# Kernel optimization log

Measured on AMD Instinct MI355X. Metric: run time of the kernel, lower is better.

The kernel has to match this reference:

```python
import jax, jax.numpy as jnp
import numpy as np

B, T, D, H, E, TOPK = 4, 1024, 1024, 16, 8, 2
DH = D // H
FF = 4 * D
EPS = 1e-9


def setup_inputs() -> dict:
    key = jax.random.key(0)
    ks = jax.random.split(key, 8)
    s = 0.02
    return {
        "x": jax.random.normal(ks[0], (B, T, D), jnp.float32),
        "c": jax.random.normal(ks[1], (B, 1, D), jnp.float32),
        "ln1_w": jnp.ones((D,), jnp.float32),
        "w_qkv": jax.random.normal(ks[2], (3 * D, D), jnp.float32) * s,
        "w_proj": jax.random.normal(ks[3], (D, D), jnp.float32) * s,
        "ln2_w": jnp.ones((D,), jnp.float32),
        "router_w": jax.random.normal(ks[4], (E, D), jnp.float32) * s,
        "expert_w1": jax.random.normal(ks[5], (E, FF, D), jnp.float32) * s,
        "expert_w2": jax.random.normal(ks[6], (E, D, FF), jnp.float32) * s,
    }


def _layernorm(x, w):
    mu = jnp.mean(x, axis=-1, keepdims=True)
    var = jnp.mean(jnp.square(x - mu), axis=-1, keepdims=True)
    return (x - mu) * jax.lax.rsqrt(var + 1e-5) * w


def reference(x, c, ln1_w, w_qkv, w_proj, ln2_w, router_w, expert_w1, expert_w2):
    # --- causal self-attention with AdaLN-style additive conditioning ---
    h = _layernorm(x, ln1_w) + c                          # [B,T,D]
    qkv = jnp.einsum('btd,ed->bte', h, w_qkv)             # [B,T,3D]
    q, k, v = jnp.split(qkv, 3, axis=-1)
    q = q.reshape(B, T, H, DH).transpose(0, 2, 1, 3)       # [B,H,T,dh]
    k = k.reshape(B, T, H, DH).transpose(0, 2, 1, 3)
    v = v.reshape(B, T, H, DH).transpose(0, 2, 1, 3)
    scores = jnp.einsum('bhqd,bhkd->bhqk', q, k) / jnp.sqrt(jnp.float32(DH))
    causal = jnp.tril(jnp.ones((T, T), bool))
    scores = jnp.where(causal, scores, jnp.float32(-1e30))
    attn = jax.nn.softmax(scores, axis=-1)
    o = jnp.einsum('bhqk,bhkd->bhqd', attn, v)
    o = o.transpose(0, 2, 1, 3).reshape(B, T, D)
    x = x + jnp.einsum('btd,ed->bte', o, w_proj)

    # --- pre-MoE LayerNorm (note: module overwrites x with ln_2(x)) ---
    x = _layernorm(x, ln2_w)

    # --- router (non-cond path): linear, max-shift, softmax, eps clamp, top-k ---
    logits = jnp.einsum('btd,ed->bte', x, router_w)        # [B,T,E]
    logits = logits - jnp.max(logits, axis=-1, keepdims=True)
    probs = jax.nn.softmax(logits, axis=-1)
    probs = jnp.clip(probs + EPS, EPS, 1.0 - EPS)
    _, top_idx = jax.lax.top_k(probs, TOPK)                # [B,T,k]
    mask = jnp.sum(jax.nn.one_hot(top_idx, E, dtype=probs.dtype), axis=-2)  # [B,T,E]
    router_probs = mask * probs
    router_probs = router_probs / jnp.sum(router_probs, axis=-1, keepdims=True)

    # --- experts: GPT MLP per expert (fc -> GELU -> proj), combine by probs ---
    # Dense-compute form is mathematically identical: router_probs is 0 for
    # non-selected experts, so masked gather/scatter == weighted dense sum.
    hid = jax.nn.gelu(jnp.einsum('btd,efd->btef', x, expert_w1), approximate=False)
    expert_out = jnp.einsum('btef,edf->bted', hid, expert_w2)  # [B,T,E,D]
    next_states = jnp.einsum('bted,bte->btd', expert_out, router_probs)

    return x + next_states
```

## Files before the change

kernel.cpp:

```cpp
#include <hip/hip_runtime.h>
#include <cstdint>
#include <cstddef>


#define AS1 __attribute__((address_space(1)))
#define AS3 __attribute__((address_space(3)))

typedef unsigned short u16;
typedef __attribute__((ext_vector_type(8))) short short8;
typedef __attribute__((ext_vector_type(8))) _Float16 half8;
typedef __attribute__((ext_vector_type(4))) float f32x4;

constexpr int Bc = 4, Tc = 1024, Dc = 1024, Hc = 16, Ec = 8, FFc = 4096;
constexpr int Mtok = Bc * Tc;

constexpr size_t PS_WQKV = (size_t)3 * Dc * Dc;
constexpr size_t PS_WPROJ = (size_t)Dc * Dc;
constexpr size_t PS_H = (size_t)Mtok * Dc;

constexpr float LO_SCALE = 4096.0f;
constexpr float LO_INV = 1.0f / 4096.0f;

__device__ __forceinline__ u16 f2bf(float f) {
  unsigned u = __float_as_uint(f);
  u += 0x7fffu + ((u >> 16) & 1u);
  return (u16)(u >> 16);
}
__device__ __forceinline__ float bf2f(u16 v) { return __uint_as_float(((unsigned)v) << 16); }
__device__ __forceinline__ u16 f2h(float f) {
  _Float16 h = (_Float16)f;
  return *(u16*)&h;
}
__device__ __forceinline__ float h2f(u16 v) {
  _Float16 h = *(_Float16*)&v;
  return (float)h;
}
__device__ __forceinline__ float gelu_f(float v) {
  return 0.5f * v * (1.0f + erff(v * 0.70710678118654752440f));
}

__global__ __launch_bounds__(256) void cvt_fp16_kernel(const float* __restrict__ in,
                                                       u16* __restrict__ out, int n4) {
  int i = blockIdx.x * 256 + threadIdx.x;
  if (i >= n4) return;
  float4 v = reinterpret_cast<const float4*>(in)[i];
  uint2 o;
  o.x = (unsigned)f2h(v.x) | ((unsigned)f2h(v.y) << 16);
  o.y = (unsigned)f2h(v.z) | ((unsigned)f2h(v.w) << 16);
  reinterpret_cast<uint2*>(out)[i] = o;
}

__global__ __launch_bounds__(256) void split2h_kernel(const float* __restrict__ in,
                                                      u16* __restrict__ out,
                                                      size_t ps, int n4) {
  int i = blockIdx.x * 256 + threadIdx.x;
  if (i >= n4) return;
  float4 v = reinterpret_cast<const float4*>(in)[i];
  float a[4] = {v.x, v.y, v.z, v.w};
  unsigned h[4], lo[4];
#pragma unroll
  for (int j = 0; j < 4; ++j) {
    u16 hh = f2h(a[j]);
    float r = (a[j] - h2f(hh)) * LO_SCALE;
    h[j] = hh; lo[j] = f2h(r);
  }
  uint2 o0, o1;
  o0.x = h[0] | (h[1] << 16);   o0.y = h[2] | (h[3] << 16);
  o1.x = lo[0] | (lo[1] << 16); o1.y = lo[2] | (lo[3] << 16);
  const size_t base = (size_t)i * 4;
  *(uint2*)&out[base] = o0;
  *(uint2*)&out[ps + base] = o1;
}

__global__ __launch_bounds__(256) void ln1_kernel(const float* __restrict__ x,
                                                  const float* __restrict__ w,
                                                  const float* __restrict__ c,
                                                  u16* __restrict__ hp) {
  const int row = blockIdx.x, tid = threadIdx.x;
  const int b = row >> 10;
  const float4 v = reinterpret_cast<const float4*>(x + (size_t)row * Dc)[tid];
  __shared__ float red[256];
  red[tid] = v.x + v.y + v.z + v.w;
  __syncthreads();
  for (int s = 128; s > 0; s >>= 1) { if (tid < s) red[tid] += red[tid + s]; __syncthreads(); }
  const float mu = red[0] * (1.0f / Dc);
  __syncthreads();
  const float dx = v.x - mu, dy = v.y - mu, dz = v.z - mu, dw = v.w - mu;
  red[tid] = dx * dx + dy * dy + dz * dz + dw * dw;
  __syncthreads();
  for (int s = 128; s > 0; s >>= 1) { if (tid < s) red[tid] += red[tid + s]; __syncthreads(); }
  const float rs = rsqrtf(red[0] * (1.0f / Dc) + 1e-5f);
  const float4 wv = reinterpret_cast<const float4*>(w)[tid];
  const float4 cv = reinterpret_cast<const float4*>(c + (size_t)b * Dc)[tid];
  float a[4];
  a[0] = dx * rs * wv.x + cv.x; a[1] = dy * rs * wv.y + cv.y;
  a[2] = dz * rs * wv.z + cv.z; a[3] = dw * rs * wv.w + cv.w;
  unsigned h[4], lo[4];
#pragma unroll
  for (int j = 0; j < 4; ++j) {
    u16 hh = f2h(a[j]);
    float r = (a[j] - h2f(hh)) * LO_SCALE;
    h[j] = hh; lo[j] = f2h(r);
  }
  uint2 o0, o1;
  o0.x = h[0] | (h[1] << 16);   o0.y = h[2] | (h[3] << 16);
  o1.x = lo[0] | (lo[1] << 16); o1.y = lo[2] | (lo[3] << 16);
  const size_t base = (size_t)row * Dc + tid * 4;
  *(uint2*)&hp[base] = o0;
  *(uint2*)&hp[PS_H + base] = o1;
}

__global__ __launch_bounds__(256) void ln2_kernel(const float* __restrict__ xin,
                                                  const float* __restrict__ w,
                                                  float* __restrict__ xf,
                                                  u16* __restrict__ xb) {
  const int row = blockIdx.x, tid = threadIdx.x;
  const float4 v = reinterpret_cast<const float4*>(xin + (size_t)row * Dc)[tid];
  __shared__ float red[256];
  red[tid] = v.x + v.y + v.z + v.w;
  __syncthreads();
  for (int s = 128; s > 0; s >>= 1) { if (tid < s) red[tid] += red[tid + s]; __syncthreads(); }
  const float mu = red[0] * (1.0f / Dc);
  __syncthreads();
  const float dx = v.x - mu, dy = v.y - mu, dz = v.z - mu, dw = v.w - mu;
  red[tid] = dx * dx + dy * dy + dz * dz + dw * dw;
  __syncthreads();
  for (int s = 128; s > 0; s >>= 1) { if (tid < s) red[tid] += red[tid + s]; __syncthreads(); }
  const float rs = rsqrtf(red[0] * (1.0f / Dc) + 1e-5f);
  const float4 wv = reinterpret_cast<const float4*>(w)[tid];
  float4 ov;
  ov.x = dx * rs * wv.x; ov.y = dy * rs * wv.y; ov.z = dz * rs * wv.z; ov.w = dw * rs * wv.w;
  reinterpret_cast<float4*>(xf + (size_t)row * Dc)[tid] = ov;
  uint2 o;
  o.x = (unsigned)f2h(ov.x) | ((unsigned)f2h(ov.y) << 16);
  o.y = (unsigned)f2h(ov.z) | ((unsigned)f2h(ov.w) << 16);
  reinterpret_cast<uint2*>(xb + (size_t)row * Dc)[tid] = o;
}

__device__ __forceinline__ void gemm_f16_core(const u16* a0, const u16* a1,
                                              const u16* b0, const u16* b1,
                                              int K, u16* As, u16* Bs, f32x4 acc[4][4]) {
  const int tid = threadIdx.x;
  const int lane = tid & 63;
  const int wave = tid >> 6;
  const int wm = (wave & 1) * 64;
  const int wn = (wave >> 1) * 64;
  const int frow = lane & 15;
  const int gs = (((lane >> 4) ^ (frow & 3))) * 8;
  int aoff[4], boff[4];
#pragma unroll
  for (int t = 0; t < 4; ++t) {
    aoff[t] = (wm + t * 16 + frow) * 32 + gs;
    boff[t] = (wn + t * 16 + frow) * 32 + gs;
  }
  const int lds0 = tid * 8;
  for (int k0 = 0; k0 < K; k0 += 32) {
    __builtin_amdgcn_global_load_lds((AS1 void*)a0, (AS3 void*)(As + lds0), 16, 0, 0);
    __builtin_amdgcn_global_load_lds((AS1 void*)a1, (AS3 void*)(As + 2048 + lds0), 16, 0, 0);
    __builtin_amdgcn_global_load_lds((AS1 void*)b0, (AS3 void*)(Bs + lds0), 16, 0, 0);
    __builtin_amdgcn_global_load_lds((AS1 void*)b1, (AS3 void*)(Bs + 2048 + lds0), 16, 0, 0);
    a0 += 32; a1 += 32; b0 += 32; b1 += 32;
    __syncthreads();
    half8 af[4], bfr[4];
#pragma unroll
    for (int t = 0; t < 4; ++t) af[t] = *(const half8*)(As + aoff[t]);
#pragma unroll
    for (int t = 0; t < 4; ++t) bfr[t] = *(const half8*)(Bs + boff[t]);
#pragma unroll
    for (int mt = 0; mt < 4; ++mt)
#pragma unroll
      for (int nt = 0; nt < 4; ++nt)
        acc[mt][nt] = __builtin_amdgcn_mfma_f32_16x16x32_f16(af[mt], bfr[nt], acc[mt][nt], 0, 0, 0);
    __syncthreads();
  }
}

__device__ __forceinline__ void gemm_f16s2_core(const u16* ah0, const u16* ah1,
                                                const u16* al0, const u16* al1,
                                                const u16* bh0, const u16* bh1,
                                                const u16* bl0, const u16* bl1,
                                                int K, u16* S,
                                                f32x4 acc0[4][4], f32x4 acc1[4][4]) {
  const int tid = threadIdx.x;
  const int lane = tid & 63;
  const int wave = tid >> 6;
  const int wm = (wave & 1) * 64;
  const int wn = (wave >> 1) * 64;
  const int frow = lane & 15;
  const int gs = (((lane >> 4) ^ (frow & 3))) * 8;
  int aoff[4], boff[4];
#pragma unroll
  for (int t = 0; t < 4; ++t) {
    aoff[t] = (wm + t * 16 + frow) * 32 + gs;
    boff[t] = (wn + t * 16 + frow) * 32 + gs;
  }
  const int lds0 = tid * 8;
  for (int k0 = 0; k0 < K; k0 += 32) {
    __builtin_amdgcn_global_load_lds((AS1 void*)ah0, (AS3 void*)(S + lds0), 16, 0, 0);
    __builtin_amdgcn_global_load_lds((AS1 void*)ah1, (AS3 void*)(S + 2048 + lds0), 16, 0, 0);
    __builtin_amdgcn_global_load_lds((AS1 void*)al0, (AS3 void*)(S + 4096 + lds0), 16, 0, 0);
    __builtin_amdgcn_global_load_lds((AS1 void*)al1, (AS3 void*)(S + 6144 + lds0), 16, 0, 0);
    __builtin_amdgcn_global_load_lds((AS1 void*)bh0, (AS3 void*)(S + 8192 + lds0), 16, 0, 0);
    __builtin_amdgcn_global_load_lds((AS1 void*)bh1, (AS3 void*)(S + 10240 + lds0), 16, 0, 0);
    __builtin_amdgcn_global_load_lds((AS1 void*)bl0, (AS3 void*)(S + 12288 + lds0), 16, 0, 0);
    __builtin_amdgcn_global_load_lds((AS1 void*)bl1, (AS3 void*)(S + 14336 + lds0), 16, 0, 0);
    ah0 += 32; ah1 += 32; al0 += 32; al1 += 32;
    bh0 += 32; bh1 += 32; bl0 += 32; bl1 += 32;
    __syncthreads();
    half8 ahf[4], bhf[4];
#pragma unroll
    for (int t = 0; t < 4; ++t) {
      ahf[t] = *(const half8*)(S + aoff[t]);
      bhf[t] = *(const half8*)(S + 8192 + boff[t]);
    }
#pragma unroll
    for (int mt = 0; mt < 4; ++mt)
#pragma unroll
      for (int nt = 0; nt < 4; ++nt)
        acc0[mt][nt] = __builtin_amdgcn_mfma_f32_16x16x32_f16(ahf[mt], bhf[nt], acc0[mt][nt], 0, 0, 0);
    {
      half8 alf[4];
#pragma unroll
      for (int t = 0; t < 4; ++t) alf[t] = *(const half8*)(S + 4096 + aoff[t]);
#pragma unroll
      for (int mt = 0; mt < 4; ++mt)
#pragma unroll
        for (int nt = 0; nt < 4; ++nt)
          acc1[mt][nt] = __builtin_amdgcn_mfma_f32_16x16x32_f16(alf[mt], bhf[nt], acc1[mt][nt], 0, 0, 0);
    }
    {
      half8 blf[4];
#pragma unroll
      for (int t = 0; t < 4; ++t) blf[t] = *(const half8*)(S + 12288 + boff[t]);
#pragma unroll
      for (int mt = 0; mt < 4; ++mt)
#pragma unroll
        for (int nt = 0; nt < 4; ++nt)
          acc1[mt][nt] = __builtin_amdgcn_mfma_f32_16x16x32_f16(ahf[mt], blf[nt], acc1[mt][nt], 0, 0, 0);
    }
    __syncthreads();
  }
}

__global__ __launch_bounds__(256) void gemm_qkv_kernel(const u16* __restrict__ A,
                                                       const u16* __restrict__ Bw,
                                                       float* __restrict__ Cout) {
  __shared__ u16 S[4 * 4096];
  const int bn = blockIdx.x, bm = blockIdx.y, tid = threadIdx.x;
  const int r = tid >> 2, kk = ((tid & 3) ^ (r & 3)) * 8;
  const u16* ah0 = A + (size_t)(bm * 128 + r) * 1024 + kk;
  const u16* ah1 = ah0 + (size_t)64 * 1024;
  const u16* bh0 = Bw + (size_t)(bn * 128 + r) * 1024 + kk;
  const u16* bh1 = bh0 + (size_t)64 * 1024;
  f32x4 acc0[4][4] = {}, acc1[4][4] = {};
  gemm_f16s2_core(ah0, ah1, ah0 + PS_H, ah1 + PS_H,
                  bh0, bh1, bh0 + PS_WQKV, bh1 + PS_WQKV,
                  1024, S, acc0, acc1);
  const int lane = tid & 63, wave = tid >> 6;
  const int wm = (wave & 1) * 64, wn = (wave >> 1) * 64;
  const int col = lane & 15, rb = (lane >> 4) * 4;
#pragma unroll
  for (int mt = 0; mt < 4; ++mt)
#pragma unroll
    for (int rr = 0; rr < 4; ++rr) {
      const int m = bm * 128 + wm + mt * 16 + rb + rr;
#pragma unroll
      for (int nt = 0; nt < 4; ++nt) {
        const int n = bn * 128 + wn + nt * 16 + col;
        Cout[(size_t)m * 3072 + n] = acc0[mt][nt][rr] + acc1[mt][nt][rr] * LO_INV;
      }
    }
}

__global__ __launch_bounds__(256) void gemm_proj_kernel(const u16* __restrict__ A,
                                                        const u16* __restrict__ Bw,
                                                        const float* __restrict__ xres,
                                                        float* __restrict__ xmid) {
  __shared__ u16 S[4 * 4096];
  const int bn = blockIdx.x, bm = blockIdx.y, tid = threadIdx.x;
  const int r = tid >> 2, kk = ((tid & 3) ^ (r & 3)) * 8;
  const u16* ah0 = A + (size_t)(bm * 128 + r) * 1024 + kk;
  const u16* ah1 = ah0 + (size_t)64 * 1024;
  const u16* bh0 = Bw + (size_t)(bn * 128 + r) * 1024 + kk;
  const u16* bh1 = bh0 + (size_t)64 * 1024;
  f32x4 acc0[4][4] = {}, acc1[4][4] = {};
  gemm_f16s2_core(ah0, ah1, ah0 + PS_H, ah1 + PS_H,
                  bh0, bh1, bh0 + PS_WPROJ, bh1 + PS_WPROJ,
                  1024, S, acc0, acc1);
  const int lane = tid & 63, wave = tid >> 6;
  const int wm = (wave & 1) * 64, wn = (wave >> 1) * 64;
  const int col = lane & 15, rb = (lane >> 4) * 4;
#pragma unroll
  for (int mt = 0; mt < 4; ++mt)
#pragma unroll
    for (int rr = 0; rr < 4; ++rr) {
      const int m = bm * 128 + wm + mt * 16 + rb + rr;
#pragma unroll
      for (int nt = 0; nt < 4; ++nt) {
        const int n = bn * 128 + wn + nt * 16 + col;
        xmid[(size_t)m * 1024 + n] =
            xres[(size_t)m * 1024 + n] + acc0[mt][nt][rr] + acc1[mt][nt][rr] * LO_INV;
      }
    }
}

__global__ __launch_bounds__(256, 3) void attn_mfma_kernel(const float* __restrict__ qkv,
                                                           float* __restrict__ obuf) {
  constexpr int KS = 72;
  constexpr int PSt = 68;
  __shared__ u16 Kh[64 * KS], Klo[64 * KS];
  __shared__ u16 Vh[64 * KS], Vlo[64 * KS];
  __shared__ u16 Ph[4][16 * PSt], Pl[4][16 * PSt];

  const int tid = threadIdx.x, lane = tid & 63, w = tid >> 6;
  const int lr = lane & 15, g = lane >> 4;
  const int bh = blockIdx.y, b = bh >> 4, h = bh & 15;
  const int blk = blockIdx.x;
  const int qrow = blk * 64 + w * 16 + lr;

  short8 qh[2], ql[2];
  {
    const float* qp = qkv + (size_t)(b * Tc + qrow) * 3072 + h * 64 + g * 8;
    const float4 f0 = *(const float4*)(qp);
    const float4 f1 = *(const float4*)(qp + 4);
    const float4 f2 = *(const float4*)(qp + 32);
    const float4 f3 = *(const float4*)(qp + 36);
    const float qq[16] = {f0.x, f0.y, f0.z, f0.w, f1.x, f1.y, f1.z, f1.w,
                          f2.x, f2.y, f2.z, f2.w, f3.x, f3.y, f3.z, f3.w};
#pragma unroll
    for (int s = 0; s < 2; ++s)
#pragma unroll
      for (int j = 0; j < 8; ++j) {
        const float v = qq[s * 8 + j] * 0.125f;
        const u16 hi = f2bf(v);
        qh[s][j] = (short)hi;
        ql[s][j] = (short)f2bf(v - bf2f(hi));
      }
  }

  const int tkl = (tid & 31) * 2;
  const int td0 = (tid >> 5) * 8;
  const float* kgb = qkv + (size_t)b * Tc * 3072 + 1024 + h * 64;
  const float* vgb = kgb + 1024;

  f32x4 oacc[4] = {};
  float mrun = -1e30f, lrun = 0.f;

  for (int c = 0; c <= blk; ++c) {
    const int k0 = c * 64;
    __syncthreads();
    {
      const float* kr0 = kgb + (size_t)(k0 + tkl) * 3072 + td0;
      const float* kr1 = kr0 + 3072;
      const float* vr0 = vgb + (size_t)(k0 + tkl) * 3072 + td0;
      const float* vr1 = vr0 + 3072;
      const float4 ka0 = *(const float4*)kr0, ka1 = *(const float4*)(kr0 + 4);
      const float4 kb0 = *(const float4*)kr1, kb1 = *(const float4*)(kr1 + 4);
      const float4 va0 = *(const float4*)vr0, va1 = *(const float4*)(vr0 + 4);
      const float4 vb0 = *(const float4*)vr1, vb1 = *(const float4*)(vr1 + 4);
      const float ka[8] = {ka0.x, ka0.y, ka0.z, ka0.w, ka1.x, ka1.y, ka1.z, ka1.w};
      const float kb[8] = {kb0.x, kb0.y, kb0.z, kb0.w, kb1.x, kb1.y, kb1.z, kb1.w};
      const float va[8] = {va0.x, va0.y, va0.z, va0.w, va1.x, va1.y, va1.z, va1.w};
      const float vb[8] = {vb0.x, vb0.y, vb0.z, vb0.w, vb1.x, vb1.y, vb1.z, vb1.w};
      short8 kh0, kl0, kh1, kl1;
#pragma unroll
      for (int j = 0; j < 8; ++j) {
        const u16 h0 = f2bf(ka[j]); kh0[j] = (short)h0; kl0[j] = (short)f2bf(ka[j] - bf2f(h0));
        const u16 h1 = f2bf(kb[j]); kh1[j] = (short)h1; kl1[j] = (short)f2bf(kb[j] - bf2f(h1));
      }
      *(short8*)(Kh + tkl * KS + td0) = kh0;
      *(short8*)(Kh + (tkl + 1) * KS + td0) = kh1;
      *(short8*)(Klo + tkl * KS + td0) = kl0;
      *(short8*)(Klo + (tkl + 1) * KS + td0) = kl1;
#pragma unroll
      for (int i = 0; i < 8; ++i) {
        const u16 h0 = f2bf(va[i]); const u16 l0 = f2bf(va[i] - bf2f(h0));
        const u16 h1 = f2bf(vb[i]); const u16 l1 = f2bf(vb[i] - bf2f(h1));
        *(unsigned*)(Vh + (td0 + i) * KS + tkl) = (unsigned)h0 | ((unsigned)h1 << 16);
        *(unsigned*)(Vlo + (td0 + i) * KS + tkl) = (unsigned)l0 | ((unsigned)l1 << 16);
      }
    }
    __syncthreads();

    f32x4 sacc[4] = {};
#pragma unroll
    for (int kt = 0; kt < 4; ++kt) {
      const u16* kap = Kh + (kt * 16 + lr) * KS + g * 8;
      const u16* klp = Klo + (kt * 16 + lr) * KS + g * 8;
      const short8 ah0 = *(const short8*)kap;
      const short8 ah1 = *(const short8*)(kap + 32);
      const short8 al0 = *(const short8*)klp;
      const short8 al1 = *(const short8*)(klp + 32);
      sacc[kt] = __builtin_amdgcn_mfma_f32_16x16x32_bf16(ah0, qh[0], sacc[kt], 0, 0, 0);
      sacc[kt] = __builtin_amdgcn_mfma_f32_16x16x32_bf16(al0, qh[0], sacc[kt], 0, 0, 0);
      sacc[kt] = __builtin_amdgcn_mfma_f32_16x16x32_bf16(ah0, ql[0], sacc[kt], 0, 0, 0);
      sacc[kt] = __builtin_amdgcn_mfma_f32_16x16x32_bf16(ah1, qh[1], sacc[kt], 0, 0, 0);
      sacc[kt] = __builtin_amdgcn_mfma_f32_16x16x32_bf16(al1, qh[1], sacc[kt], 0, 0, 0);
      sacc[kt] = __builtin_amdgcn_mfma_f32_16x16x32_bf16(ah1, ql[1], sacc[kt], 0, 0, 0);
    }

    if (c == blk) {
#pragma unroll
      for (int kt = 0; kt < 4; ++kt)
#pragma unroll
        for (int r = 0; r < 4; ++r)
          if (k0 + kt * 16 + g * 4 + r > qrow) sacc[kt][r] = -1e30f;
    }

    float mt = -1e30f;
#pragma unroll
    for (int kt = 0; kt < 4; ++kt)
#pragma unroll
      for (int r = 0; r < 4; ++r) mt = fmaxf(mt, sacc[kt][r]);
    mt = fmaxf(mt, __shfl_xor(mt, 16));
    mt = fmaxf(mt, __shfl_xor(mt, 32));
    const float mnew = fmaxf(mrun, mt);
    const float alpha = __expf(mrun - mnew);
    float psum = 0.f;
    u16* php = Ph[w] + lr * PSt;
    u16* plp = Pl[w] + lr * PSt;
#pragma unroll
    for (int kt = 0; kt < 4; ++kt) {
      u16 hh[4], ll[4];
#pragma unroll
      for (int r = 0; r < 4; ++r) {
        const float p = __expf(sacc[kt][r] - mnew);
        psum += p;
        hh[r] = f2bf(p);
        ll[r] = f2bf(p - bf2f(hh[r]));
      }
      uint2 wh, wl;
      wh.x = (unsigned)hh[0] | ((unsigned)hh[1] << 16);
      wh.y = (unsigned)hh[2] | ((unsigned)hh[3] << 16);
      wl.x = (unsigned)ll[0] | ((unsigned)ll[1] << 16);
      wl.y = (unsigned)ll[2] | ((unsigned)ll[3] << 16);
      *(uint2*)(php + kt * 16 + g * 4) = wh;
      *(uint2*)(plp + kt * 16 + g * 4) = wl;
    }
    psum += __shfl_xor(psum, 16);
    psum += __shfl_xor(psum, 32);
    mrun = mnew;
    lrun = lrun * alpha + psum;
#pragma unroll
    for (int dt = 0; dt < 4; ++dt) {
      oacc[dt][0] *= alpha; oacc[dt][1] *= alpha;
      oacc[dt][2] *= alpha; oacc[dt][3] *= alpha;
    }
    __syncthreads();

    const short8 pbh0 = *(const short8*)(php + g * 8);
    const short8 pbh1 = *(const short8*)(php + 32 + g * 8);
    const short8 pbl0 = *(const short8*)(plp + g * 8);
    const short8 pbl1 = *(const short8*)(plp + 32 + g * 8);
#pragma unroll
    for (int dt = 0; dt < 4; ++dt) {
      const u16* vap = Vh + (dt * 16 + lr) * KS + g * 8;
      const u16* vlp2 = Vlo + (dt * 16 + lr) * KS + g * 8;
      const short8 vh0 = *(const short8*)vap;
      const short8 vh1 = *(const short8*)(vap + 32);
      const short8 vl0 = *(const short8*)vlp2;
      const short8 vl1 = *(const short8*)(vlp2 + 32);
      oacc[dt] = __builtin_amdgcn_mfma_f32_16x16x32_bf16(vh0, pbh0, oacc[dt], 0, 0, 0);
      oacc[dt] = __builtin_amdgcn_mfma_f32_16x16x32_bf16(vl0, pbh0, oacc[dt], 0, 0, 0);
      oacc[dt] = __builtin_amdgcn_mfma_f32_16x16x32_bf16(vh0, pbl0, oacc[dt], 0, 0, 0);
      oacc[dt] = __builtin_amdgcn_mfma_f32_16x16x32_bf16(vh1, pbh1, oacc[dt], 0, 0, 0);
      oacc[dt] = __builtin_amdgcn_mfma_f32_16x16x32_bf16(vl1, pbh1, oacc[dt], 0, 0, 0);
      oacc[dt] = __builtin_amdgcn_mfma_f32_16x16x32_bf16(vh1, pbl1, oacc[dt], 0, 0, 0);
    }
  }

  const float invl = 1.0f / lrun;
  float* ob = obuf + (size_t)(b * Tc + qrow) * 1024 + h * 64;
#pragma unroll
  for (int dt = 0; dt < 4; ++dt) {
    float4 o4;
    o4.x = oacc[dt][0] * invl; o4.y = oacc[dt][1] * invl;
    o4.z = oacc[dt][2] * invl; o4.w = oacc[dt][3] * invl;
    *(float4*)(ob + dt * 16 + g * 4) = o4;
  }
}

__global__ __launch_bounds__(256) void router_kernel(const float* __restrict__ x2,
                                                     const float* __restrict__ rw,
                                                     int* __restrict__ cnt,
                                                     int* __restrict__ tok,
                                                     float* __restrict__ wt) {
  __shared__ float xr[1024];
  __shared__ float part[8][32];
  __shared__ float lg[8];
  const int row = blockIdx.x, tid = threadIdx.x;
  reinterpret_cast<float4*>(xr)[tid] = reinterpret_cast<const float4*>(x2 + (size_t)row * Dc)[tid];
  __syncthreads();
  const int e = tid >> 5, j = tid & 31;
  float p = 0.f;
  for (int d = j; d < Dc; d += 32) p += xr[d] * rw[e * Dc + d];
  part[e][j] = p;
  __syncthreads();
  if (tid < 8) {
    float s = 0.f;
    for (int q = 0; q < 32; ++q) s += part[tid][q];
    lg[tid] = s;
  }
  __syncthreads();
  if (tid == 0) {
    int i0 = 0;
    for (int q = 1; q < 8; ++q) if (lg[q] > lg[i0]) i0 = q;
    int i1 = (i0 == 0) ? 1 : 0;
    for (int q = 0; q < 8; ++q) if (q != i0 && lg[q] > lg[i1]) i1 = q;
    float mx = lg[0];
    for (int q = 1; q < 8; ++q) mx = fmaxf(mx, lg[q]);
    float ex[8], s = 0.f;
    for (int q = 0; q < 8; ++q) { ex[q] = expf(lg[q] - mx); s += ex[q]; }
    const float inv = 1.f / s;
    float p0v = fminf(fmaxf(ex[i0] * inv + 1e-9f, 1e-9f), 1.f - 1e-9f);
    float p1v = fminf(fmaxf(ex[i1] * inv + 1e-9f, 1e-9f), 1.f - 1e-9f);
    const float sw = 1.f / (p0v + p1v);
    int p0 = atomicAdd(&cnt[i0], 1);
    tok[i0 * Mtok + p0] = row; wt[i0 * Mtok + p0] = p0v * sw;
    int p1 = atomicAdd(&cnt[i1], 1);
    tok[i1 * Mtok + p1] = row; wt[i1 * Mtok + p1] = p1v * sw;
  }
}

__global__ __launch_bounds__(256) void gemm_e1_kernel(const u16* __restrict__ x2b,
                                                      const u16* __restrict__ w1,
                                                      const int* __restrict__ cnt,
                                                      const int* __restrict__ tok,
                                                      u16* __restrict__ hid) {
  const int bn = blockIdx.x;
  const int e = blockIdx.y >> 5, it = blockIdx.y & 31;
  const int n_e = cnt[e];
  if (it * 128 >= n_e) return;
  int offs = 0;
  for (int q = 0; q < 8; ++q) offs += (q < e) ? cnt[q] : 0;
  __shared__ u16 As[128 * 32], Bs[128 * 32];
  const int tid = threadIdx.x;
  const int r = tid >> 2, kk = ((tid & 3) ^ (r & 3)) * 8;
  const int i0 = it * 128 + r, i1 = i0 + 64;
  const int t0 = tok[e * Mtok + ((i0 < n_e) ? i0 : (n_e - 1))];
  const int t1 = tok[e * Mtok + ((i1 < n_e) ? i1 : (n_e - 1))];
  const u16* a0 = x2b + (size_t)t0 * 1024 + kk;
  const u16* a1 = x2b + (size_t)t1 * 1024 + kk;
  const u16* b0 = w1 + (size_t)e * FFc * Dc + (size_t)(bn * 128 + r) * 1024 + kk;
  const u16* b1 = b0 + (size_t)64 * 1024;
  f32x4 acc[4][4] = {};
  gemm_f16_core(a0, a1, b0, b1, 1024, As, Bs, acc);
  const int lane = tid & 63, wave = tid >> 6;
  const int wm = (wave & 1) * 64, wn = (wave >> 1) * 64;
  const int col = lane & 15, rb = (lane >> 4) * 4;
#pragma unroll
  for (int mt = 0; mt < 4; ++mt)
#pragma unroll
    for (int rr = 0; rr < 4; ++rr) {
      const int i = it * 128 + wm + mt * 16 + rb + rr;
      if (i < n_e) {
        const size_t hrow = (size_t)(offs + i) * FFc;
#pragma unroll
        for (int nt = 0; nt < 4; ++nt) {
          const int n = bn * 128 + wn + nt * 16 + col;
          hid[hrow + n] = f2h(gelu_f(acc[mt][nt][rr]));
        }
      }
    }
}

__global__ __launch_bounds__(256) void gemm_e2_kernel(const u16* __restrict__ hid,
                                                      const u16* __restrict__ w2,
                                                      const int* __restrict__ cnt,
                                                      const int* __restrict__ tok,
                                                      const float* __restrict__ wt,
                                                      float* __restrict__ out) {
  const int bn = blockIdx.x;
  const int e = blockIdx.y >> 5, it = blockIdx.y & 31;
  const int n_e = cnt[e];
  if (it * 128 >= n_e) return;
  int offs = 0;
  for (int q = 0; q < 8; ++q) offs += (q < e) ? cnt[q] : 0;
  __shared__ u16 As[128 * 32], Bs[128 * 32];
  const int tid = threadIdx.x;
  const int r = tid >> 2, kk = ((tid & 3) ^ (r & 3)) * 8;
  const int i0 = it * 128 + r, i1 = i0 + 64;
  const int ri0 = offs + ((i0 < n_e) ? i0 : (n_e - 1));
  const int ri1 = offs + ((i1 < n_e) ? i1 : (n_e - 1));
  const u16* a0 = hid + (size_t)ri0 * FFc + kk;
  const u16* a1 = hid + (size_t)ri1 * FFc + kk;
  const u16* b0 = w2 + (size_t)e * Dc * FFc + (size_t)(bn * 128 + r) * FFc + kk;
  const u16* b1 = b0 + (size_t)64 * FFc;
  f32x4 acc[4][4] = {};
  gemm_f16_core(a0, a1, b0, b1, FFc, As, Bs, acc);
  const int lane = tid & 63, wave = tid >> 6;
  const int wm = (wave & 1) * 64, wn = (wave >> 1) * 64;
  const int col = lane & 15, rb = (lane >> 4) * 4;
#pragma unroll
  for (int mt = 0; mt < 4; ++mt)
#pragma unroll
    for (int rr = 0; rr < 4; ++rr) {
      const int i = it * 128 + wm + mt * 16 + rb + rr;
      if (i < n_e) {
        const int tk = tok[e * Mtok + i];
        const float wgt = wt[e * Mtok + i];
#pragma unroll
        for (int nt = 0; nt < 4; ++nt) {
          const int n = bn * 128 + wn + nt * 16 + col;
          atomicAdd(&out[(size_t)tk * 1024 + n], wgt * acc[mt][nt][rr]);
        }
      }
    }
}

constexpr size_t OFF_WQKV3 = 0;
constexpr size_t OFF_WPROJ3 = 18874368;
constexpr size_t OFF_W1 = 25165824;
constexpr size_t OFF_W2 = 92274688;
constexpr size_t OFF_HPL = 159383552;
constexpr size_t OFF_QKV = 184549376;
constexpr size_t OFF_OF = 234881024;
constexpr size_t OFF_X2 = 251658240;
constexpr size_t OFF_CNT = 260046848;
constexpr size_t OFF_TOK = OFF_CNT + 256;
constexpr size_t OFF_WTL = OFF_TOK + (size_t)Ec * Mtok * 4;

extern "C" void kernel_launch(void* const* d_in, const int* in_sizes, int n_in,
                              void* d_out, int out_size, void* d_ws, size_t ws_size,
                              hipStream_t stream) {
  const float* x = (const float*)d_in[0];
  const float* c = (const float*)d_in[1];
  const float* ln1_w = (const float*)d_in[2];
  const float* w_qkv = (const float*)d_in[3];
  const float* w_proj = (const float*)d_in[4];
  const float* ln2_w = (const float*)d_in[5];
  const float* router_w = (const float*)d_in[6];
  const float* ew1 = (const float*)d_in[7];
  const float* ew2 = (const float*)d_in[8];
  float* out = (float*)d_out;
  char* ws = (char*)d_ws;

  u16* wqkv2 = (u16*)(ws + OFF_WQKV3);
  u16* wproj2 = (u16*)(ws + OFF_WPROJ3);
  u16* w1_h = (u16*)(ws + OFF_W1);
  u16* w2_h = (u16*)(ws + OFF_W2);
  u16* hpl = (u16*)(ws + OFF_HPL);
  float* qkvf = (float*)(ws + OFF_QKV);
  float* of = (float*)(ws + OFF_OF);
  u16* x2_h = (u16*)(ws + OFF_X2);
  u16* hid_h = (u16*)(ws + OFF_QKV);
  int* cnt = (int*)(ws + OFF_CNT);
  int* tok = (int*)(ws + OFF_TOK);
  float* wtl = (float*)(ws + OFF_WTL);

  split2h_kernel<<<(3 * Dc * Dc / 4 + 255) / 256, 256, 0, stream>>>(w_qkv, wqkv2, PS_WQKV, 3 * Dc * Dc / 4);
  split2h_kernel<<<(Dc * Dc / 4 + 255) / 256, 256, 0, stream>>>(w_proj, wproj2, PS_WPROJ, Dc * Dc / 4);
  {
    int n4 = Ec * FFc * Dc / 4;
    cvt_fp16_kernel<<<(n4 + 255) / 256, 256, 0, stream>>>(ew1, w1_h, n4);
    cvt_fp16_kernel<<<(n4 + 255) / 256, 256, 0, stream>>>(ew2, w2_h, n4);
  }
  ln1_kernel<<<Mtok, 256, 0, stream>>>(x, ln1_w, c, hpl);
  gemm_qkv_kernel<<<dim3(24, 32), 256, 0, stream>>>(hpl, wqkv2, qkvf);
  attn_mfma_kernel<<<dim3(Tc / 64, Bc * Hc), 256, 0, stream>>>(qkvf, of);
  split2h_kernel<<<(Mtok * Dc / 4 + 255) / 256, 256, 0, stream>>>(of, hpl, PS_H, Mtok * Dc / 4);
  gemm_proj_kernel<<<dim3(8, 32), 256, 0, stream>>>(hpl, wproj2, x, of);
  ln2_kernel<<<Mtok, 256, 0, stream>>>(of, ln2_w, out, x2_h);
  (void)hipMemsetAsync(cnt, 0, Ec * sizeof(int), stream);
  router_kernel<<<Mtok, 256, 0, stream>>>(out, router_w, cnt, tok, wtl);
  gemm_e1_kernel<<<dim3(32, 256), 256, 0, stream>>>(x2_h, w1_h, cnt, tok, hid_h);
  gemm_e2_kernel<<<dim3(8, 256), 256, 0, stream>>>(hid_h, w2_h, cnt, tok, wtl, out);
}
```

Baseline: 1.032 ms.

## Double-buffer LDS tiles in GEMM cores and change the LDS swizzle pattern

The GEMM main loops now prefetch the next K-slice into a second LDS buffer with global_load_lds while MFMAs run on the current one, dropping one barrier per iteration. The XOR swizzle moves from row&3 to (row>>1)&3, intended to cut LDS bank conflicts on fragment reads. LDS use per block doubles, which can lower occupancy, and the single barrier per iteration has to order both the prefetch writes and the reads of the other buffer correctly.

```diff
diff --git a/kernel.cpp b/kernel.cpp
--- a/kernel.cpp
+++ b/kernel.cpp
@@ -137,41 +137,67 @@
   reinterpret_cast<uint2*>(xb + (size_t)row * Dc)[tid] = o;
 }
 
+__device__ __forceinline__ void stage4(const u16* a0, const u16* a1,
+                                       const u16* b0, const u16* b1,
+                                       u16* buf, int lds0) {
+  __builtin_amdgcn_global_load_lds((AS1 void*)a0, (AS3 void*)(buf + lds0), 16, 0, 0);
+  __builtin_amdgcn_global_load_lds((AS1 void*)a1, (AS3 void*)(buf + 2048 + lds0), 16, 0, 0);
+  __builtin_amdgcn_global_load_lds((AS1 void*)b0, (AS3 void*)(buf + 4096 + lds0), 16, 0, 0);
+  __builtin_amdgcn_global_load_lds((AS1 void*)b1, (AS3 void*)(buf + 6144 + lds0), 16, 0, 0);
+}
+__device__ __forceinline__ void stage8(const u16* ah0, const u16* ah1,
+                                       const u16* al0, const u16* al1,
+                                       const u16* bh0, const u16* bh1,
+                                       const u16* bl0, const u16* bl1,
+                                       u16* buf, int lds0) {
+  __builtin_amdgcn_global_load_lds((AS1 void*)ah0, (AS3 void*)(buf + lds0), 16, 0, 0);
+  __builtin_amdgcn_global_load_lds((AS1 void*)ah1, (AS3 void*)(buf + 2048 + lds0), 16, 0, 0);
+  __builtin_amdgcn_global_load_lds((AS1 void*)al0, (AS3 void*)(buf + 4096 + lds0), 16, 0, 0);
+  __builtin_amdgcn_global_load_lds((AS1 void*)al1, (AS3 void*)(buf + 6144 + lds0), 16, 0, 0);
+  __builtin_amdgcn_global_load_lds((AS1 void*)bh0, (AS3 void*)(buf + 8192 + lds0), 16, 0, 0);
+  __builtin_amdgcn_global_load_lds((AS1 void*)bh1, (AS3 void*)(buf + 10240 + lds0), 16, 0, 0);
+  __builtin_amdgcn_global_load_lds((AS1 void*)bl0, (AS3 void*)(buf + 12288 + lds0), 16, 0, 0);
+  __builtin_amdgcn_global_load_lds((AS1 void*)bl1, (AS3 void*)(buf + 14336 + lds0), 16, 0, 0);
+}
+
 __device__ __forceinline__ void gemm_f16_core(const u16* a0, const u16* a1,
                                               const u16* b0, const u16* b1,
-                                              int K, u16* As, u16* Bs, f32x4 acc[4][4]) {
+                                              int K, u16* S, f32x4 acc[4][4]) {
   const int tid = threadIdx.x;
   const int lane = tid & 63;
   const int wave = tid >> 6;
   const int wm = (wave & 1) * 64;
   const int wn = (wave >> 1) * 64;
   const int frow = lane & 15;
-  const int gs = (((lane >> 4) ^ (frow & 3))) * 8;
+  const int gs = ((lane >> 4) ^ ((frow >> 1) & 3)) * 8;
   int aoff[4], boff[4];
 #pragma unroll
   for (int t = 0; t < 4; ++t) {
     aoff[t] = (wm + t * 16 + frow) * 32 + gs;
-    boff[t] = (wn + t * 16 + frow) * 32 + gs;
+    boff[t] = 4096 + (wn + t * 16 + frow) * 32 + gs;
   }
   const int lds0 = tid * 8;
+  stage4(a0, a1, b0, b1, S, lds0);
+  a0 += 32; a1 += 32; b0 += 32; b1 += 32;
+  int cur = 0;
   for (int k0 = 0; k0 < K; k0 += 32) {
-    __builtin_amdgcn_global_load_lds((AS1 void*)a0, (AS3 void*)(As + lds0), 16, 0, 0);
-    __builtin_amdgcn_global_load_lds((AS1 void*)a1, (AS3 void*)(As + 2048 + lds0), 16, 0, 0);
-    __builtin_amdgcn_global_load_lds((AS1 void*)b0, (AS3 void*)(Bs + lds0), 16, 0, 0);
-    __builtin_amdgcn_global_load_lds((AS1 void*)b1, (AS3 void*)(Bs + 2048 + lds0), 16, 0, 0);
-    a0 += 32; a1 += 32; b0 += 32; b1 += 32;
     __syncthreads();
+    if (k0 + 32 < K) {
+      stage4(a0, a1, b0, b1, S + (cur ^ 1) * 8192, lds0);
+      a0 += 32; a1 += 32; b0 += 32; b1 += 32;
+    }
+    const u16* As = S + cur * 8192;
     half8 af[4], bfr[4];
 #pragma unroll
     for (int t = 0; t < 4; ++t) af[t] = *(const half8*)(As + aoff[t]);
 #pragma unroll
-    for (int t = 0; t < 4; ++t) bfr[t] = *(const half8*)(Bs + boff[t]);
+    for (int t = 0; t < 4; ++t) bfr[t] = *(const half8*)(As + boff[t]);
 #pragma unroll
     for (int mt = 0; mt < 4; ++mt)
 #pragma unroll
       for (int nt = 0; nt < 4; ++nt)
         acc[mt][nt] = __builtin_amdgcn_mfma_f32_16x16x32_f16(af[mt], bfr[nt], acc[mt][nt], 0, 0, 0);
-    __syncthreads();
+    cur ^= 1;
   }
 }
 
@@ -187,31 +213,31 @@
   const int wm = (wave & 1) * 64;
   const int wn = (wave >> 1) * 64;
   const int frow = lane & 15;
-  const int gs = (((lane >> 4) ^ (frow & 3))) * 8;
+  const int gs = ((lane >> 4) ^ ((frow >> 1) & 3)) * 8;
   int aoff[4], boff[4];
 #pragma unroll
   for (int t = 0; t < 4; ++t) {
     aoff[t] = (wm + t * 16 + frow) * 32 + gs;
-    boff[t] = (wn + t * 16 + frow) * 32 + gs;
+    boff[t] = 8192 + (wn + t * 16 + frow) * 32 + gs;
   }
   const int lds0 = tid * 8;
+  stage8(ah0, ah1, al0, al1, bh0, bh1, bl0, bl1, S, lds0);
+  ah0 += 32; ah1 += 32; al0 += 32; al1 += 32;
+  bh0 += 32; bh1 += 32; bl0 += 32; bl1 += 32;
+  int cur = 0;
   for (int k0 = 0; k0 < K; k0 += 32) {
-    __builtin_amdgcn_global_load_lds((AS1 void*)ah0, (AS3 void*)(S + lds0), 16, 0, 0);
-    __builtin_amdgcn_global_load_lds((AS1 void*)ah1, (AS3 void*)(S + 2048 + lds0), 16, 0, 0);
-    __builtin_amdgcn_global_load_lds((AS1 void*)al0, (AS3 void*)(S + 4096 + lds0), 16, 0, 0);
-    __builtin_amdgcn_global_load_lds((AS1 void*)al1, (AS3 void*)(S + 6144 + lds0), 16, 0, 0);
-    __builtin_amdgcn_global_load_lds((AS1 void*)bh0, (AS3 void*)(S + 8192 + lds0), 16, 0, 0);
-    __builtin_amdgcn_global_load_lds((AS1 void*)bh1, (AS3 void*)(S + 10240 + lds0), 16, 0, 0);
-    __builtin_amdgcn_global_load_lds((AS1 void*)bl0, (AS3 void*)(S + 12288 + lds0), 16, 0, 0);
-    __builtin_amdgcn_global_load_lds((AS1 void*)bl1, (AS3 void*)(S + 14336 + lds0), 16, 0, 0);
-    ah0 += 32; ah1 += 32; al0 += 32; al1 += 32;
-    bh0 += 32; bh1 += 32; bl0 += 32; bl1 += 32;
     __syncthreads();
+    if (k0 + 32 < K) {
+      stage8(ah0, ah1, al0, al1, bh0, bh1, bl0, bl1, S + (cur ^ 1) * 16384, lds0);
+      ah0 += 32; ah1 += 32; al0 += 32; al1 += 32;
+      bh0 += 32; bh1 += 32; bl0 += 32; bl1 += 32;
+    }
+    const u16* Sb = S + cur * 16384;
     half8 ahf[4], bhf[4];
 #pragma unroll
     for (int t = 0; t < 4; ++t) {
-      ahf[t] = *(const half8*)(S + aoff[t]);
-      bhf[t] = *(const half8*)(S + 8192 + boff[t]);
+      ahf[t] = *(const half8*)(Sb + aoff[t]);
+      bhf[t] = *(const half8*)(Sb + boff[t]);
     }
 #pragma unroll
     for (int mt = 0; mt < 4; ++mt)
@@ -221,7 +247,7 @@
     {
       half8 alf[4];
 #pragma unroll
-      for (int t = 0; t < 4; ++t) alf[t] = *(const half8*)(S + 4096 + aoff[t]);
+      for (int t = 0; t < 4; ++t) alf[t] = *(const half8*)(Sb + 4096 + aoff[t]);
 #pragma unroll
       for (int mt = 0; mt < 4; ++mt)
 #pragma unroll
@@ -231,23 +257,23 @@
     {
       half8 blf[4];
 #pragma unroll
-      for (int t = 0; t < 4; ++t) blf[t] = *(const half8*)(S + 12288 + boff[t]);
+      for (int t = 0; t < 4; ++t) blf[t] = *(const half8*)(Sb + 4096 + boff[t]);
 #pragma unroll
       for (int mt = 0; mt < 4; ++mt)
 #pragma unroll
         for (int nt = 0; nt < 4; ++nt)
           acc1[mt][nt] = __builtin_amdgcn_mfma_f32_16x16x32_f16(ahf[mt], blf[nt], acc1[mt][nt], 0, 0, 0);
     }
-    __syncthreads();
+    cur ^= 1;
   }
 }
 
 __global__ __launch_bounds__(256) void gemm_qkv_kernel(const u16* __restrict__ A,
                                                        const u16* __restrict__ Bw,
                                                        float* __restrict__ Cout) {
-  __shared__ u16 S[4 * 4096];
+  __shared__ u16 S[2 * 16384];
   const int bn = blockIdx.x, bm = blockIdx.y, tid = threadIdx.x;
-  const int r = tid >> 2, kk = ((tid & 3) ^ (r & 3)) * 8;
+  const int r = tid >> 2, kk = ((tid & 3) ^ ((r >> 1) & 3)) * 8;
   const u16* ah0 = A + (size_t)(bm * 128 + r) * 1024 + kk;
   const u16* ah1 = ah0 + (size_t)64 * 1024;
   const u16* bh0 = Bw + (size_t)(bn * 128 + r) * 1024 + kk;
@@ -276,9 +302,9 @@
                                                         const u16* __restrict__ Bw,
                                                         const float* __restrict__ xres,
                                                         float* __restrict__ xmid) {
-  __shared__ u16 S[4 * 4096];
+  __shared__ u16 S[2 * 16384];
   const int bn = blockIdx.x, bm = blockIdx.y, tid = threadIdx.x;
-  const int r = tid >> 2, kk = ((tid & 3) ^ (r & 3)) * 8;
+  const int r = tid >> 2, kk = ((tid & 3) ^ ((r >> 1) & 3)) * 8;
   const u16* ah0 = A + (size_t)(bm * 128 + r) * 1024 + kk;
   const u16* ah1 = ah0 + (size_t)64 * 1024;
   const u16* bh0 = Bw + (size_t)(bn * 128 + r) * 1024 + kk;
@@ -533,9 +559,9 @@
   if (it * 128 >= n_e) return;
   int offs = 0;
   for (int q = 0; q < 8; ++q) offs += (q < e) ? cnt[q] : 0;
-  __shared__ u16 As[128 * 32], Bs[128 * 32];
+  __shared__ u16 S[2 * 8192];
   const int tid = threadIdx.x;
-  const int r = tid >> 2, kk = ((tid & 3) ^ (r & 3)) * 8;
+  const int r = tid >> 2, kk = ((tid & 3) ^ ((r >> 1) & 3)) * 8;
   const int i0 = it * 128 + r, i1 = i0 + 64;
   const int t0 = tok[e * Mtok + ((i0 < n_e) ? i0 : (n_e - 1))];
   const int t1 = tok[e * Mtok + ((i1 < n_e) ? i1 : (n_e - 1))];
@@ -544,7 +570,7 @@
   const u16* b0 = w1 + (size_t)e * FFc * Dc + (size_t)(bn * 128 + r) * 1024 + kk;
   const u16* b1 = b0 + (size_t)64 * 1024;
   f32x4 acc[4][4] = {};
-  gemm_f16_core(a0, a1, b0, b1, 1024, As, Bs, acc);
+  gemm_f16_core(a0, a1, b0, b1, 1024, S, acc);
   const int lane = tid & 63, wave = tid >> 6;
   const int wm = (wave & 1) * 64, wn = (wave >> 1) * 64;
   const int col = lane & 15, rb = (lane >> 4) * 4;
@@ -576,9 +602,9 @@
   if (it * 128 >= n_e) return;
   int offs = 0;
   for (int q = 0; q < 8; ++q) offs += (q < e) ? cnt[q] : 0;
-  __shared__ u16 As[128 * 32], Bs[128 * 32];
+  __shared__ u16 S[2 * 8192];
   const int tid = threadIdx.x;
-  const int r = tid >> 2, kk = ((tid & 3) ^ (r & 3)) * 8;
+  const int r = tid >> 2, kk = ((tid & 3) ^ ((r >> 1) & 3)) * 8;
   const int i0 = it * 128 + r, i1 = i0 + 64;
   const int ri0 = offs + ((i0 < n_e) ? i0 : (n_e - 1));
   const int ri1 = offs + ((i1 < n_e) ? i1 : (n_e - 1));
@@ -587,7 +613,7 @@
   const u16* b0 = w2 + (size_t)e * Dc * FFc + (size_t)(bn * 128 + r) * FFc + kk;
   const u16* b1 = b0 + (size_t)64 * FFc;
   f32x4 acc[4][4] = {};
-  gemm_f16_core(a0, a1, b0, b1, FFc, As, Bs, acc);
+  gemm_f16_core(a0, a1, b0, b1, FFc, S, acc);
   const int lane = tid & 63, wave = tid >> 6;
   const int wm = (wave & 1) * 64, wn = (wave >> 1) * 64;
   const int col = lane & 15, rb = (lane >> 4) * 4;
```

Result: faster. 943.5 us (-8.6%).
